# Kernel optimization log

Measured on AMD Instinct MI355X. Metric: run time of the kernel, lower is better.

Reference implementation:

```python
import jax, jax.numpy as jnp
import numpy as np

EMBED_DIM = 1024
N_HEAD = 16

def setup_inputs() -> dict:
    key = jax.random.key(0)
    ks = jax.random.split(key, 5)
    C = EMBED_DIM
    x = jax.random.normal(ks[0], (2, 2048, C), dtype=jnp.float32)
    s = 1.0 / np.sqrt(C)
    W_attn = jax.random.normal(ks[1], (C, 3 * C), dtype=jnp.float32) * s
    b_attn = jnp.zeros((3 * C,), dtype=jnp.float32)
    W_proj = jax.random.normal(ks[2], (C, C), dtype=jnp.float32) * s
    b_proj = jnp.zeros((C,), dtype=jnp.float32)
    return {"x": x, "W_attn": W_attn, "b_attn": b_attn, "W_proj": W_proj, "b_proj": b_proj}

def reference(x, W_attn, b_attn, W_proj, b_proj):
    B, T, C = x.shape
    H = N_HEAD
    D = C // H
    qkv = x @ W_attn + b_attn                      # [B,T,3C]
    q, k, v = jnp.split(qkv, 3, axis=-1)
    # [B,H,T,D]
    q = q.reshape(B, T, H, D).transpose(0, 2, 1, 3)
    k = k.reshape(B, T, H, D).transpose(0, 2, 1, 3)
    v = v.reshape(B, T, H, D).transpose(0, 2, 1, 3)
    att = jnp.einsum('bhqd,bhkd->bhqk', q, k) * (1.0 / jnp.sqrt(jnp.asarray(D, x.dtype)))
    causal = jnp.tril(jnp.ones((T, T), dtype=bool))
    att = jnp.where(causal, att, -jnp.inf)
    att = jax.nn.softmax(att, axis=-1)
    y = jnp.einsum('bhqk,bhkd->bhqd', att, v)      # [B,H,T,D]
    y = y.transpose(0, 2, 1, 3).reshape(B, T, C)
    return y @ W_proj + b_proj
```

## Files before the change

kernel.cpp:

```cpp
#include <hip/hip_runtime.h>
#include <stdint.h>

typedef __attribute__((ext_vector_type(4))) float f32x4;
typedef __attribute__((ext_vector_type(8))) __bf16 bf16x8;
typedef __attribute__((ext_vector_type(8))) unsigned short u16x8;

__device__ __forceinline__ unsigned short f2b(float f) {
  unsigned u = __float_as_uint(f);
  u += 0x7FFFu + ((u >> 16) & 1u);
  return (unsigned short)(u >> 16);
}
__device__ __forceinline__ float b2f(unsigned short s) {
  unsigned u = (unsigned)s << 16;
  return __uint_as_float(u);
}

__device__ __forceinline__ void gload_lds16(const void* g, void* l) {
  typedef __attribute__((address_space(1))) void GV1;
  typedef __attribute__((address_space(3))) void LV3;
  __builtin_amdgcn_global_load_lds((GV1*)(void*)g, (LV3*)l, 16, 0, 0);
}

__global__ __launch_bounds__(256) void convert_f32_bf16(const float* __restrict__ in,
                                                        unsigned short* __restrict__ out, int n) {
  int i = (blockIdx.x * 256 + threadIdx.x) * 8;
  if (i >= n) return;
  float4 a = *(const float4*)(in + i);
  float4 b = *(const float4*)(in + i + 4);
  u16x8 r;
  r[0] = f2b(a.x); r[1] = f2b(a.y); r[2] = f2b(a.z); r[3] = f2b(a.w);
  r[4] = f2b(b.x); r[5] = f2b(b.y); r[6] = f2b(b.z); r[7] = f2b(b.w);
  *(u16x8*)(out + i) = r;
}

__global__ __launch_bounds__(256) void transpose_f32_bf16(const float* __restrict__ W,
                                                          unsigned short* __restrict__ Wt,
                                                          int K, int N) {
  __shared__ unsigned short tile[32][33];
  int n0 = blockIdx.x * 32, k0 = blockIdx.y * 32;
  int tx = threadIdx.x, ty = threadIdx.y;
  #pragma unroll
  for (int j = 0; j < 32; j += 8)
    tile[ty + j][tx] = f2b(W[(size_t)(k0 + ty + j) * N + n0 + tx]);
  __syncthreads();
  #pragma unroll
  for (int j = 0; j < 32; j += 8)
    Wt[(size_t)(n0 + ty + j) * K + k0 + tx] = tile[tx][ty + j];
}

template <bool OUT_BF16>
__global__ __launch_bounds__(256) void gemm_bt(const unsigned short* __restrict__ A,
                                               const unsigned short* __restrict__ Bt,
                                               const float* __restrict__ bias,
                                               void* __restrict__ Cout,
                                               int M, int N, int K) {
  __shared__ unsigned short As[128 * 64];
  __shared__ unsigned short Bs[128 * 64];
  const int m0 = blockIdx.x * 128, n0 = blockIdx.y * 128;
  const int tid = threadIdx.x;
  const int w = tid >> 6, l = tid & 63;
  const int wm = w >> 1, wn = w & 1;
  const int c = l & 15, g = l >> 4;
  f32x4 acc[4][4] = {};
  for (int k0 = 0; k0 < K; k0 += 64) {
    #pragma unroll
    for (int i = 0; i < 4; ++i) {
      int rb = w * 32 + i * 8;
      gload_lds16(A + (size_t)(m0 + rb + (l >> 3)) * K + k0 + (l & 7) * 8, &As[rb * 64]);
      gload_lds16(Bt + (size_t)(n0 + rb + (l >> 3)) * K + k0 + (l & 7) * 8, &Bs[rb * 64]);
    }
    __syncthreads();
    #pragma unroll
    for (int ks = 0; ks < 2; ++ks) {
      bf16x8 af[4], bf[4];
      #pragma unroll
      for (int mi = 0; mi < 4; ++mi)
        af[mi] = *(const bf16x8*)&As[(wm * 64 + mi * 16 + c) * 64 + ks * 32 + g * 8];
      #pragma unroll
      for (int ni = 0; ni < 4; ++ni)
        bf[ni] = *(const bf16x8*)&Bs[(wn * 64 + ni * 16 + c) * 64 + ks * 32 + g * 8];
      #pragma unroll
      for (int mi = 0; mi < 4; ++mi)
        #pragma unroll
        for (int ni = 0; ni < 4; ++ni)
          acc[mi][ni] = __builtin_amdgcn_mfma_f32_16x16x32_bf16(af[mi], bf[ni], acc[mi][ni], 0, 0, 0);
    }
    __syncthreads();
  }
  #pragma unroll
  for (int mi = 0; mi < 4; ++mi) {
    #pragma unroll
    for (int ni = 0; ni < 4; ++ni) {
      int colg = n0 + wn * 64 + ni * 16 + c;
      float bv = bias[colg];
      #pragma unroll
      for (int r = 0; r < 4; ++r) {
        int rowg = m0 + wm * 64 + mi * 16 + 4 * g + r;
        float v = acc[mi][ni][r] + bv;
        if (OUT_BF16)
          ((unsigned short*)Cout)[(size_t)rowg * N + colg] = f2b(v);
        else
          ((float*)Cout)[(size_t)rowg * N + colg] = v;
      }
    }
  }
}

__global__ __launch_bounds__(256) void attn_kernel(const unsigned short* __restrict__ qkv,
                                                   unsigned short* __restrict__ partO,
                                                   float* __restrict__ partML) {
  __shared__ unsigned short K_lds[2][64 * 64];
  __shared__ unsigned short V_lds[2][64 * 64];
  __shared__ unsigned short P_lds[4 * 16 * 64];
  const int bid = blockIdx.x;
  const int bh = bid & 31;
  const int cid = bid >> 5;
  int qt, ct;
  if (cid < 32)      { qt = cid;      ct = 0; }
  else if (cid < 56) { qt = cid - 24; ct = 1; }
  else if (cid < 72) { qt = cid - 40; ct = 2; }
  else               { qt = cid - 48; ct = 3; }
  const int t0 = ct * 8;
  const int ntl = min(qt + 1 - t0, 8);
  const bool hasdiag = (t0 + ntl - 1) == qt;
  const int b = bh >> 4, h = bh & 15;
  const int tid = threadIdx.x, w = tid >> 6, l = tid & 63;
  const int c = l & 15, g = l >> 4;
  const size_t row0 = (size_t)b * 2048;
  const int vp = tid & 31, vcb = tid >> 5;
  const float SCL = 0.18033688f;
  char* Pb = (char*)&P_lds[w * 16 * 64];

  const int q0w = qt * 64 + w * 16;

  bf16x8 qf[2];
  #pragma unroll
  for (int ks = 0; ks < 2; ++ks)
    qf[ks] = *(const bf16x8*)(qkv + (row0 + q0w + c) * 3072 + h * 64 + ks * 32 + g * 8);

  f32x4 acc[4] = {};
  float mstate[4], lstate[4];
  #pragma unroll
  for (int r = 0; r < 4; ++r) { mstate[r] = -1e30f; lstate[r] = 0.f; }

  {
    #pragma unroll
    for (int i = 0; i < 2; ++i) {
      int rb = w * 16 + i * 8;
      int row = rb + (l >> 3);
      int ch = (l & 7) ^ (row & 7);
      gload_lds16(qkv + (row0 + t0 * 64 + row) * 3072 + 1024 + h * 64 + ch * 8,
                  &K_lds[0][rb * 64]);
    }
    size_t tr = row0 + t0 * 64 + 2 * vp;
    u16x8 v0 = *(const u16x8*)(qkv + tr * 3072 + 2048 + h * 64 + vcb * 8);
    u16x8 v1 = *(const u16x8*)(qkv + (tr + 1) * 3072 + 2048 + h * 64 + vcb * 8);
    char* Vb = (char*)V_lds[0];
    #pragma unroll
    for (int jj = 0; jj < 8; ++jj) {
      int d = vcb * 8 + jj;
      int off = d * 128 + ((4 * vp) ^ ((d & 7) << 4));
      *(unsigned int*)(Vb + off) = (unsigned int)v0[jj] | ((unsigned int)v1[jj] << 16);
    }
  }
  __syncthreads();

  for (int lt = 0; lt < ntl; ++lt) {
    const int cur = lt & 1;
    const int kv0 = (t0 + lt) * 64;
    const bool pre = (lt + 1 < ntl);
    u16x8 v0n, v1n;
    if (pre) {
      const int kvn = kv0 + 64;
      #pragma unroll
      for (int ii = 0; ii < 2; ++ii) {
        int rb = w * 16 + ii * 8;
        int row = rb + (l >> 3);
        int ch = (l & 7) ^ (row & 7);
        gload_lds16(qkv + (row0 + kvn + row) * 3072 + 1024 + h * 64 + ch * 8,
                    &K_lds[cur ^ 1][rb * 64]);
      }
      size_t tr = row0 + kvn + 2 * vp;
      v0n = *(const u16x8*)(qkv + tr * 3072 + 2048 + h * 64 + vcb * 8);
      v1n = *(const u16x8*)(qkv + (tr + 1) * 3072 + 2048 + h * 64 + vcb * 8);
    }
    const char* Kb = (const char*)K_lds[cur];
    const char* Vb = (const char*)V_lds[cur];
    f32x4 s[4] = {};
    #pragma unroll
    for (int ks = 0; ks < 2; ++ks) {
      bf16x8 kf[4];
      #pragma unroll
      for (int nk = 0; nk < 4; ++nk) {
        int row = nk * 16 + c;
        kf[nk] = *(const bf16x8*)(Kb + row * 128 + ((ks * 64 + g * 16) ^ ((row & 7) << 4)));
      }
      __builtin_amdgcn_s_setprio(1);
      #pragma unroll
      for (int nk = 0; nk < 4; ++nk)
        s[nk] = __builtin_amdgcn_mfma_f32_16x16x32_bf16(qf[ks], kf[nk], s[nk], 0, 0, 0);
      __builtin_amdgcn_s_setprio(0);
    }
    if (hasdiag && lt == ntl - 1) {
      #pragma unroll
      for (int nk = 0; nk < 4; ++nk)
        #pragma unroll
        for (int r = 0; r < 4; ++r) {
          int rowg = q0w + 4 * g + r;
          int colg = kv0 + nk * 16 + c;
          if (colg > rowg) s[nk][r] = -1e30f;
        }
    }
    float mx[4];
    #pragma unroll
    for (int r = 0; r < 4; ++r) {
      float m0 = fmaxf(fmaxf(s[0][r], s[1][r]), fmaxf(s[2][r], s[3][r]));
      m0 = fmaxf(m0, __shfl_xor(m0, 1));
      m0 = fmaxf(m0, __shfl_xor(m0, 2));
      m0 = fmaxf(m0, __shfl_xor(m0, 4));
      m0 = fmaxf(m0, __shfl_xor(m0, 8));
      mx[r] = m0;
    }
    bool nogrow = (mx[0] <= mstate[0]) & (mx[1] <= mstate[1]) &
                  (mx[2] <= mstate[2]) & (mx[3] <= mstate[3]);
    if (!__all(nogrow)) {
      #pragma unroll
      for (int r = 0; r < 4; ++r) {
        float mold = mstate[r];
        float mnew = fmaxf(mold, mx[r]);
        float alpha = exp2f((mold - mnew) * SCL);
        mstate[r] = mnew;
        lstate[r] *= alpha;
        #pragma unroll
        for (int nd = 0; nd < 4; ++nd) acc[nd][r] *= alpha;
      }
    }
    #pragma unroll
    for (int r = 0; r < 4; ++r) {
      float ms = mstate[r] * SCL;
      float p0 = exp2f(fmaf(s[0][r], SCL, -ms));
      float p1 = exp2f(fmaf(s[1][r], SCL, -ms));
      float p2 = exp2f(fmaf(s[2][r], SCL, -ms));
      float p3 = exp2f(fmaf(s[3][r], SCL, -ms));
      s[0][r] = p0; s[1][r] = p1; s[2][r] = p2; s[3][r] = p3;
      lstate[r] += (p0 + p1) + (p2 + p3);
    }
    #pragma unroll
    for (int nk = 0; nk < 4; ++nk)
      #pragma unroll
      for (int r = 0; r < 4; ++r) {
        int row = 4 * g + r;
        int off = row * 128 + (((nk * 16 + c) * 2) ^ ((row & 7) << 4));
        *(unsigned short*)(Pb + off) = f2b(s[nk][r]);
      }
    #pragma unroll
    for (int ks = 0; ks < 2; ++ks) {
      bf16x8 pf, vf[4];
      pf = *(const bf16x8*)(Pb + c * 128 + ((ks * 64 + g * 16) ^ ((c & 7) << 4)));
      #pragma unroll
      for (int nd = 0; nd < 4; ++nd) {
        int row = nd * 16 + c;
        vf[nd] = *(const bf16x8*)(Vb + row * 128 + ((ks * 64 + g * 16) ^ ((row & 7) << 4)));
      }
      __builtin_amdgcn_s_setprio(1);
      #pragma unroll
      for (int nd = 0; nd < 4; ++nd)
        acc[nd] = __builtin_amdgcn_mfma_f32_16x16x32_bf16(pf, vf[nd], acc[nd], 0, 0, 0);
      __builtin_amdgcn_s_setprio(0);
    }
    if (pre) {
      char* Vbn = (char*)V_lds[cur ^ 1];
      #pragma unroll
      for (int jj = 0; jj < 8; ++jj) {
        int d = vcb * 8 + jj;
        int off = d * 128 + ((4 * vp) ^ ((d & 7) << 4));
        *(unsigned int*)(Vbn + off) = (unsigned int)v0n[jj] | ((unsigned int)v1n[jj] << 16);
      }
    }
    __syncthreads();
  }

  #pragma unroll
  for (int r = 0; r < 4; ++r) {
    float ls = lstate[r];
    ls += __shfl_xor(ls, 1);
    ls += __shfl_xor(ls, 2);
    ls += __shfl_xor(ls, 4);
    ls += __shfl_xor(ls, 8);
    int row = w * 16 + 4 * g + r;
    #pragma unroll
    for (int nd = 0; nd < 4; ++nd)
      partO[(size_t)bid * 4096 + row * 64 + nd * 16 + c] = f2b(acc[nd][r]);
    if (c == 0) {
      partML[(size_t)bid * 128 + row * 2 + 0] = mstate[r];
      partML[(size_t)bid * 128 + row * 2 + 1] = ls;
    }
  }
}

__global__ __launch_bounds__(256) void attn_combine(const unsigned short* __restrict__ partO,
                                                    const float* __restrict__ partML,
                                                    unsigned short* __restrict__ out) {
  const int bid = blockIdx.x;
  const int qt = bid >> 5, bh = bid & 31;
  const int b = bh >> 4, h = bh & 15;
  const int np = (qt >> 3) + 1;
  const int t = threadIdx.x;
  const int row = t >> 2, cg = (t & 3) * 16;
  const float SCL = 0.18033688f;
  int slot0 = ((qt +  0) << 5) | bh;
  int slot1 = ((qt + 24) << 5) | bh;
  int slot2 = ((qt + 40) << 5) | bh;
  int slot3 = ((qt + 48) << 5) | bh;
  float mstar = partML[(size_t)slot0 * 128 + row * 2];
  if (np > 1) mstar = fmaxf(mstar, partML[(size_t)slot1 * 128 + row * 2]);
  if (np > 2) mstar = fmaxf(mstar, partML[(size_t)slot2 * 128 + row * 2]);
  if (np > 3) mstar = fmaxf(mstar, partML[(size_t)slot3 * 128 + row * 2]);
  float L = 0.f;
  float o[16];
  #pragma unroll
  for (int j = 0; j < 16; ++j) o[j] = 0.f;
  #pragma unroll
  for (int p = 0; p < 4; ++p) {
    if (p < np) {
      int slot = p == 0 ? slot0 : (p == 1 ? slot1 : (p == 2 ? slot2 : slot3));
      float mp = partML[(size_t)slot * 128 + row * 2 + 0];
      float lp = partML[(size_t)slot * 128 + row * 2 + 1];
      float wgt = exp2f((mp - mstar) * SCL);
      L = fmaf(wgt, lp, L);
      const unsigned short* src = partO + (size_t)slot * 4096 + row * 64 + cg;
      u16x8 a = *(const u16x8*)src;
      u16x8 bb = *(const u16x8*)(src + 8);
      #pragma unroll
      for (int j = 0; j < 8; ++j) {
        o[j]     = fmaf(b2f(a[j]),  wgt, o[j]);
        o[j + 8] = fmaf(b2f(bb[j]), wgt, o[j + 8]);
      }
    }
  }
  float rinv = 1.0f / L;
  u16x8 r0, r1;
  #pragma unroll
  for (int j = 0; j < 8; ++j) {
    r0[j] = f2b(o[j] * rinv);
    r1[j] = f2b(o[j + 8] * rinv);
  }
  size_t trow = (size_t)b * 2048 + qt * 64 + row;
  *(u16x8*)(out + trow * 1024 + h * 64 + cg) = r0;
  *(u16x8*)(out + trow * 1024 + h * 64 + cg + 8) = r1;
}

extern "C" void kernel_launch(void* const* d_in, const int* in_sizes, int n_in,
                              void* d_out, int out_size, void* d_ws, size_t ws_size,
                              hipStream_t stream) {
  const float* x      = (const float*)d_in[0];
  const float* W_attn = (const float*)d_in[1];
  const float* b_attn = (const float*)d_in[2];
  const float* W_proj = (const float*)d_in[3];
  const float* b_proj = (const float*)d_in[4];
  float* out = (float*)d_out;

  char* ws = (char*)d_ws;
  unsigned short* Wproj_t  = (unsigned short*)(ws + 0);
  unsigned short* qkv      = (unsigned short*)(ws + 2097152);
  unsigned short* x_bf     = (unsigned short*)(ws + 27262976);
  unsigned short* Wattn_t  = (unsigned short*)(ws + 35651584);
  unsigned short* partO    = (unsigned short*)(ws + 27262976);
  unsigned short* attn_out = (unsigned short*)(ws + 48234496);
  float*          partML   = (float*)(ws + 56623104);

  convert_f32_bf16<<<2048, 256, 0, stream>>>(x, x_bf, 4194304);
  transpose_f32_bf16<<<dim3(96, 32), dim3(32, 8), 0, stream>>>(W_attn, Wattn_t, 1024, 3072);
  transpose_f32_bf16<<<dim3(32, 32), dim3(32, 8), 0, stream>>>(W_proj, Wproj_t, 1024, 1024);

  gemm_bt<true><<<dim3(32, 24), 256, 0, stream>>>(x_bf, Wattn_t, b_attn, qkv, 4096, 3072, 1024);
  attn_kernel<<<2560, 256, 0, stream>>>(qkv, partO, partML);
  attn_combine<<<1024, 256, 0, stream>>>(partO, partML, attn_out);
  gemm_bt<false><<<dim3(32, 8), 256, 0, stream>>>(attn_out, Wproj_t, b_proj, out, 4096, 1024, 1024);
}
```

Baseline: 164.0 us.

## Compute transposed S and O tiles to keep P in registers via shuffles

Swaps the MFMA operand order so each lane holds a single query row's scores across the KV dimension. The softmax state becomes one scalar per lane with cheaper cross-lane reductions. P is packed to bf16 with v_cvt_pk_bf16_f32 and redistributed through lane shuffles instead of a round trip through LDS, and the per-wave P buffer is removed. Output stores become vectorized ushort4 writes. The cost is extra shuffles and selects in the PV stage, plus reliance on inline assembly.

```diff
diff --git a/kernel.cpp b/kernel.cpp
--- a/kernel.cpp
+++ b/kernel.cpp
@@ -13,6 +13,11 @@
 __device__ __forceinline__ float b2f(unsigned short s) {
   unsigned u = (unsigned)s << 16;
   return __uint_as_float(u);
+}
+__device__ __forceinline__ unsigned cvtpk_bf16(float lo, float hi) {
+  unsigned r;
+  asm("v_cvt_pk_bf16_f32 %0, %1, %2" : "=v"(r) : "v"(lo), "v"(hi));
+  return r;
 }
 
 __device__ __forceinline__ void gload_lds16(const void* g, void* l) {
@@ -111,7 +116,6 @@
                                                    float* __restrict__ partML) {
   __shared__ unsigned short K_lds[2][64 * 64];
   __shared__ unsigned short V_lds[2][64 * 64];
-  __shared__ unsigned short P_lds[4 * 16 * 64];
   const int bid = blockIdx.x;
   const int bh = bid & 31;
   const int cid = bid >> 5;
@@ -126,22 +130,23 @@
   const int b = bh >> 4, h = bh & 15;
   const int tid = threadIdx.x, w = tid >> 6, l = tid & 63;
   const int c = l & 15, g = l >> 4;
+  const int hi = g >> 1;
+  const int srcA = c + ((g & 1) << 5);
+  const int srcB = srcA + 16;
   const size_t row0 = (size_t)b * 2048;
   const int vp = tid & 31, vcb = tid >> 5;
   const float SCL = 0.18033688f;
-  char* Pb = (char*)&P_lds[w * 16 * 64];
 
   const int q0w = qt * 64 + w * 16;
+  const int qg = q0w + c;
 
   bf16x8 qf[2];
   #pragma unroll
   for (int ks = 0; ks < 2; ++ks)
-    qf[ks] = *(const bf16x8*)(qkv + (row0 + q0w + c) * 3072 + h * 64 + ks * 32 + g * 8);
+    qf[ks] = *(const bf16x8*)(qkv + (row0 + qg) * 3072 + h * 64 + ks * 32 + g * 8);
 
   f32x4 acc[4] = {};
-  float mstate[4], lstate[4];
-  #pragma unroll
-  for (int r = 0; r < 4; ++r) { mstate[r] = -1e30f; lstate[r] = 0.f; }
+  float mstate = -1e30f, lstate = 0.f;
 
   {
     #pragma unroll
@@ -198,7 +203,7 @@
       __builtin_amdgcn_s_setprio(1);
       #pragma unroll
       for (int nk = 0; nk < 4; ++nk)
-        s[nk] = __builtin_amdgcn_mfma_f32_16x16x32_bf16(qf[ks], kf[nk], s[nk], 0, 0, 0);
+        s[nk] = __builtin_amdgcn_mfma_f32_16x16x32_bf16(kf[nk], qf[ks], s[nk], 0, 0, 0);
       __builtin_amdgcn_s_setprio(0);
     }
     if (hasdiag && lt == ntl - 1) {
@@ -206,66 +211,63 @@
       for (int nk = 0; nk < 4; ++nk)
         #pragma unroll
         for (int r = 0; r < 4; ++r) {
-          int rowg = q0w + 4 * g + r;
-          int colg = kv0 + nk * 16 + c;
-          if (colg > rowg) s[nk][r] = -1e30f;
+          int kvg = kv0 + nk * 16 + 4 * g + r;
+          if (kvg > qg) s[nk][r] = -1e30f;
         }
     }
-    float mx[4];
-    #pragma unroll
-    for (int r = 0; r < 4; ++r) {
-      float m0 = fmaxf(fmaxf(s[0][r], s[1][r]), fmaxf(s[2][r], s[3][r]));
-      m0 = fmaxf(m0, __shfl_xor(m0, 1));
-      m0 = fmaxf(m0, __shfl_xor(m0, 2));
-      m0 = fmaxf(m0, __shfl_xor(m0, 4));
-      m0 = fmaxf(m0, __shfl_xor(m0, 8));
-      mx[r] = m0;
-    }
-    bool nogrow = (mx[0] <= mstate[0]) & (mx[1] <= mstate[1]) &
-                  (mx[2] <= mstate[2]) & (mx[3] <= mstate[3]);
-    if (!__all(nogrow)) {
-      #pragma unroll
-      for (int r = 0; r < 4; ++r) {
-        float mold = mstate[r];
-        float mnew = fmaxf(mold, mx[r]);
-        float alpha = exp2f((mold - mnew) * SCL);
-        mstate[r] = mnew;
-        lstate[r] *= alpha;
-        #pragma unroll
-        for (int nd = 0; nd < 4; ++nd) acc[nd][r] *= alpha;
-      }
-    }
-    #pragma unroll
-    for (int r = 0; r < 4; ++r) {
-      float ms = mstate[r] * SCL;
-      float p0 = exp2f(fmaf(s[0][r], SCL, -ms));
-      float p1 = exp2f(fmaf(s[1][r], SCL, -ms));
-      float p2 = exp2f(fmaf(s[2][r], SCL, -ms));
-      float p3 = exp2f(fmaf(s[3][r], SCL, -ms));
-      s[0][r] = p0; s[1][r] = p1; s[2][r] = p2; s[3][r] = p3;
-      lstate[r] += (p0 + p1) + (p2 + p3);
-    }
-    #pragma unroll
-    for (int nk = 0; nk < 4; ++nk)
-      #pragma unroll
-      for (int r = 0; r < 4; ++r) {
-        int row = 4 * g + r;
-        int off = row * 128 + (((nk * 16 + c) * 2) ^ ((row & 7) << 4));
-        *(unsigned short*)(Pb + off) = f2b(s[nk][r]);
-      }
-    #pragma unroll
-    for (int ks = 0; ks < 2; ++ks) {
-      bf16x8 pf, vf[4];
-      pf = *(const bf16x8*)(Pb + c * 128 + ((ks * 64 + g * 16) ^ ((c & 7) << 4)));
+    float a0 = fmaxf(fmaxf(s[0][0], s[0][1]), fmaxf(s[0][2], s[0][3]));
+    float a1 = fmaxf(fmaxf(s[1][0], s[1][1]), fmaxf(s[1][2], s[1][3]));
+    float a2 = fmaxf(fmaxf(s[2][0], s[2][1]), fmaxf(s[2][2], s[2][3]));
+    float a3 = fmaxf(fmaxf(s[3][0], s[3][1]), fmaxf(s[3][2], s[3][3]));
+    float mx = fmaxf(fmaxf(a0, a1), fmaxf(a2, a3));
+    mx = fmaxf(mx, __shfl_xor(mx, 16));
+    mx = fmaxf(mx, __shfl_xor(mx, 32));
+    if (!__all(mx <= mstate)) {
+      float mnew = fmaxf(mstate, mx);
+      float alpha = exp2f((mstate - mnew) * SCL);
+      mstate = mnew;
+      lstate *= alpha;
+      #pragma unroll
+      for (int nd = 0; nd < 4; ++nd) acc[nd] *= alpha;
+    }
+    float ms = mstate * SCL;
+    #pragma unroll
+    for (int nk = 0; nk < 4; ++nk) {
+      #pragma unroll
+      for (int r = 0; r < 4; ++r) s[nk][r] = exp2f(fmaf(s[nk][r], SCL, -ms));
+      lstate += (s[nk][0] + s[nk][1]) + (s[nk][2] + s[nk][3]);
+    }
+    unsigned pk[4][2];
+    #pragma unroll
+    for (int nk = 0; nk < 4; ++nk) {
+      pk[nk][0] = cvtpk_bf16(s[nk][0], s[nk][1]);
+      pk[nk][1] = cvtpk_bf16(s[nk][2], s[nk][3]);
+    }
+    #pragma unroll
+    for (int vks = 0; vks < 2; ++vks) {
+      unsigned rA00 = __shfl(pk[2 * vks][0], srcA, 64);
+      unsigned rA01 = __shfl(pk[2 * vks][1], srcA, 64);
+      unsigned rA10 = __shfl(pk[2 * vks + 1][0], srcA, 64);
+      unsigned rA11 = __shfl(pk[2 * vks + 1][1], srcA, 64);
+      unsigned rB00 = __shfl(pk[2 * vks][0], srcB, 64);
+      unsigned rB01 = __shfl(pk[2 * vks][1], srcB, 64);
+      unsigned rB10 = __shfl(pk[2 * vks + 1][0], srcB, 64);
+      unsigned rB11 = __shfl(pk[2 * vks + 1][1], srcB, 64);
+      union { unsigned u[4]; bf16x8 v; } pa;
+      pa.u[0] = hi ? rA10 : rA00;
+      pa.u[1] = hi ? rA11 : rA01;
+      pa.u[2] = hi ? rB10 : rB00;
+      pa.u[3] = hi ? rB11 : rB01;
+      bf16x8 vf[4];
       #pragma unroll
       for (int nd = 0; nd < 4; ++nd) {
         int row = nd * 16 + c;
-        vf[nd] = *(const bf16x8*)(Vb + row * 128 + ((ks * 64 + g * 16) ^ ((row & 7) << 4)));
+        vf[nd] = *(const bf16x8*)(Vb + row * 128 + ((vks * 64 + g * 16) ^ ((row & 7) << 4)));
       }
       __builtin_amdgcn_s_setprio(1);
       #pragma unroll
       for (int nd = 0; nd < 4; ++nd)
-        acc[nd] = __builtin_amdgcn_mfma_f32_16x16x32_bf16(pf, vf[nd], acc[nd], 0, 0, 0);
+        acc[nd] = __builtin_amdgcn_mfma_f32_16x16x32_bf16(vf[nd], pa.v, acc[nd], 0, 0, 0);
       __builtin_amdgcn_s_setprio(0);
     }
     if (pre) {
@@ -280,21 +282,20 @@
     __syncthreads();
   }
 
-  #pragma unroll
-  for (int r = 0; r < 4; ++r) {
-    float ls = lstate[r];
-    ls += __shfl_xor(ls, 1);
-    ls += __shfl_xor(ls, 2);
-    ls += __shfl_xor(ls, 4);
-    ls += __shfl_xor(ls, 8);
-    int row = w * 16 + 4 * g + r;
-    #pragma unroll
-    for (int nd = 0; nd < 4; ++nd)
-      partO[(size_t)bid * 4096 + row * 64 + nd * 16 + c] = f2b(acc[nd][r]);
-    if (c == 0) {
-      partML[(size_t)bid * 128 + row * 2 + 0] = mstate[r];
-      partML[(size_t)bid * 128 + row * 2 + 1] = ls;
-    }
+  float lsum = lstate;
+  lsum += __shfl_xor(lsum, 16);
+  lsum += __shfl_xor(lsum, 32);
+  const int qrow = w * 16 + c;
+  #pragma unroll
+  for (int nd = 0; nd < 4; ++nd) {
+    ushort4 o4;
+    o4.x = f2b(acc[nd][0]); o4.y = f2b(acc[nd][1]);
+    o4.z = f2b(acc[nd][2]); o4.w = f2b(acc[nd][3]);
+    *(ushort4*)(partO + (size_t)bid * 4096 + qrow * 64 + nd * 16 + 4 * g) = o4;
+  }
+  if (g == 0) {
+    partML[(size_t)bid * 128 + qrow * 2 + 0] = mstate;
+    partML[(size_t)bid * 128 + qrow * 2 + 1] = lsum;
   }
 }
 
```

After: 153.1 us, median of 2. -6.6%, faster.
